# Optimization experiments

Hardware: AMD Instinct MI355X
Metric: run time of the kernel (lower is better)

The kernel has to match this reference:

```python
import jax, jax.numpy as jnp
import numpy as np

B, S, D, H, DFF = 4, 1024, 1024, 16, 4096
DK = D // H
EPS = 1e-9


def _layernorm(x, alpha, bias):
    # Faithful to source: torch.std is unbiased (ddof=1), eps added to std.
    mean = jnp.mean(x, axis=-1, keepdims=True)
    xc = x - mean
    std = jnp.sqrt(jnp.sum(xc * xc, axis=-1, keepdims=True) / (x.shape[-1] - 1))
    return alpha * xc / (std + EPS) + bias


def _mha(x, wq_w, wq_b, wo_w, wo_b):
    # Source bug preserved: w_q is used for q, k, AND v projections.
    p = (x @ wq_w + wq_b).reshape(B, S, H, DK).transpose(0, 2, 1, 3)  # [B,H,S,DK]
    scores = jnp.einsum('bhqd,bhkd->bhqk', p, p) / jnp.sqrt(jnp.asarray(DK, x.dtype))
    attn = jax.nn.softmax(scores, axis=-1)
    out = jnp.einsum('bhqk,bhkd->bhqd', attn, p)
    out = out.transpose(0, 2, 1, 3).reshape(B, S, D)
    return out @ wo_w + wo_b


def _ffn(x, w1, b1, w2, b2):
    return jax.nn.relu(x @ w1 + b1) @ w2 + b2


def setup_inputs() -> dict:
    key = jax.random.key(0)
    ks = jax.random.split(key, 8)
    sc = 0.02
    return {
        'x': jax.random.normal(ks[0], (B, S, D), jnp.float32),
        'wq_w': sc * jax.random.normal(ks[1], (D, D), jnp.float32),
        'wq_b': jnp.zeros((D,), jnp.float32),
        'wo_w': sc * jax.random.normal(ks[2], (D, D), jnp.float32),
        'wo_b': jnp.zeros((D,), jnp.float32),
        'ff1_w': sc * jax.random.normal(ks[3], (D, DFF), jnp.float32),
        'ff1_b': jnp.zeros((DFF,), jnp.float32),
        'ff2_w': sc * jax.random.normal(ks[4], (DFF, D), jnp.float32),
        'ff2_b': jnp.zeros((D,), jnp.float32),
        'alpha1': jnp.ones((1,), jnp.float32), 'bias1': jnp.zeros((1,), jnp.float32),
        'alpha2': jnp.ones((1,), jnp.float32), 'bias2': jnp.zeros((1,), jnp.float32),
        'alpha3': jnp.ones((1,), jnp.float32), 'bias3': jnp.zeros((1,), jnp.float32),
    }


def reference(x, wq_w, wq_b, wo_w, wo_b, ff1_w, ff1_b, ff2_w, ff2_b,
              alpha1, bias1, alpha2, bias2, alpha3, bias3):
    h1 = x + _mha(_layernorm(x, alpha1, bias1), wq_w, wq_b, wo_w, wo_b)
    h2 = h1 + _ffn(_layernorm(h1, alpha2, bias2), ff1_w, ff1_b, ff2_w, ff2_b)
    return _layernorm(h2, alpha3, bias3)
```

## Files before the change

### kernel.cpp

```cpp
#include <hip/hip_runtime.h>

typedef short short8 __attribute__((ext_vector_type(8)));
typedef float f32x4 __attribute__((ext_vector_type(4)));
typedef unsigned short u16x4 __attribute__((ext_vector_type(4)));

#define DEV static __device__ __forceinline__

DEV float b2f(unsigned short u) { return __uint_as_float(((unsigned)u) << 16); }
DEV unsigned short f2b(float f) {
    unsigned u = __float_as_uint(f);
    u += 0x7FFFu + ((u >> 16) & 1u);
    return (unsigned short)(u >> 16);
}
DEV float wred_sum(float v) {
#pragma unroll
    for (int o = 32; o; o >>= 1) v += __shfl_xor(v, o);
    return v;
}

DEV void gld_lds16(const unsigned short* g, unsigned short* l) {
    __builtin_amdgcn_global_load_lds((const __attribute__((address_space(1))) void*)g,
                                     (__attribute__((address_space(3))) void*)l, 16, 0, 0);
}

template <bool OUT_BF16>
__global__ __launch_bounds__(256) void ln_kernel(const float* __restrict__ in,
                                                 void* __restrict__ out_v,
                                                 const float* __restrict__ alpha_p,
                                                 const float* __restrict__ bias_p) {
    __shared__ float redA[4], redB[4];
    const int row = blockIdx.x;
    const int t = threadIdx.x;
    const int lane = t & 63, w = t >> 6;

    f32x4 xv = *(const f32x4*)&in[(size_t)row * 1024 + t * 4];

    float s = wred_sum(xv[0] + xv[1] + xv[2] + xv[3]);
    if (lane == 0) redA[w] = s;
    __syncthreads();
    float mean = (redA[0] + redA[1] + redA[2] + redA[3]) * (1.0f / 1024.0f);

    float d0 = xv[0] - mean, d1 = xv[1] - mean, d2 = xv[2] - mean, d3 = xv[3] - mean;
    float ss = wred_sum(d0 * d0 + d1 * d1 + d2 * d2 + d3 * d3);
    if (lane == 0) redB[w] = ss;
    __syncthreads();
    float var = (redB[0] + redB[1] + redB[2] + redB[3]) * (1.0f / 1023.0f);
    float denom = sqrtf(var) + 1e-9f;
    float inv = alpha_p[0] / denom;
    float bias = bias_p[0];

    if (OUT_BF16) {
        u16x4 o;
        o[0] = f2b(d0 * inv + bias);
        o[1] = f2b(d1 * inv + bias);
        o[2] = f2b(d2 * inv + bias);
        o[3] = f2b(d3 * inv + bias);
        *(u16x4*)&((unsigned short*)out_v)[(size_t)row * 1024 + t * 4] = o;
    } else {
        f32x4 o;
        o[0] = d0 * inv + bias;
        o[1] = d1 * inv + bias;
        o[2] = d2 * inv + bias;
        o[3] = d3 * inv + bias;
        *(f32x4*)&((float*)out_v)[(size_t)row * 1024 + t * 4] = o;
    }
}

__global__ __launch_bounds__(256) void transpose_cast_kernel(const float* __restrict__ in,
                                                             unsigned short* __restrict__ out,
                                                             int R, int C) {
    __shared__ unsigned short tile[32][33];
    const int c0 = blockIdx.x * 32, r0 = blockIdx.y * 32;
    const int x = threadIdx.x, y0 = threadIdx.y;
#pragma unroll
    for (int yy = y0; yy < 32; yy += 8) tile[yy][x] = f2b(in[(size_t)(r0 + yy) * C + c0 + x]);
    __syncthreads();
#pragma unroll
    for (int yy = y0; yy < 32; yy += 8) out[(size_t)(c0 + yy) * R + r0 + x] = tile[x][yy];
}

__global__ __launch_bounds__(256) void transpose_bf16_batch(const unsigned short* __restrict__ in,
                                                            unsigned short* __restrict__ out) {
    __shared__ unsigned short tile[32][33];
    const int b = blockIdx.z;
    const int d0 = blockIdx.x * 32, s0 = blockIdx.y * 32;
    const unsigned short* I = in + (size_t)b * 1024 * 1024;
    unsigned short* O = out + (size_t)b * 1024 * 1024;
    const int x = threadIdx.x, y0 = threadIdx.y;
#pragma unroll
    for (int yy = y0; yy < 32; yy += 8) tile[yy][x] = I[(size_t)(s0 + yy) * 1024 + d0 + x];
    __syncthreads();
#pragma unroll
    for (int yy = y0; yy < 32; yy += 8) O[(size_t)(d0 + yy) * 1024 + s0 + x] = tile[x][yy];
}

template <int BM, int BN, bool RELU, bool RES, bool OUT_BF16>
__global__ __launch_bounds__(256) void gemm2b(const unsigned short* __restrict__ A,
                                              const unsigned short* __restrict__ Bt,
                                              const float* __restrict__ bias,
                                              const float* __restrict__ res,
                                              void* __restrict__ C_v,
                                              int M, int N, int K) {
    constexpr int WM = BM / 2, WN = BN / 2;
    constexpr int FM = WM / 16, FN = WN / 16;
    __shared__ __align__(16) unsigned short As[3][BM * 64];
    __shared__ __align__(16) unsigned short Bs[3][BN * 64];

    const int t = threadIdx.x;
    const int lane = t & 63, w = t >> 6;
    const int wr = w >> 1, wc = w & 1;
    const int lr = lane & 15, g = lane >> 4;

    const int nwg = gridDim.x;
    const int cpx = nwg >> 3;
    const int wg = blockIdx.x;
    const int swz = (wg & 7) * cpx + (wg >> 3);
    const int NB = N / BN;
    const int m0 = (swz / NB) * BM, n0 = (swz % NB) * BN;

    f32x4 acc[FM][FN];
#pragma unroll
    for (int i = 0; i < FM; ++i)
#pragma unroll
        for (int j = 0; j < FN; ++j) acc[i][j] = (f32x4)0.0f;

    const int NT = K / 64;

#define STAGE2B(kt)                                                                        \
    {                                                                                      \
        const int buf_ = (kt) % 3;                                                         \
        const int k0_ = (kt) * 64;                                                         \
        _Pragma("unroll") for (int i = 0; i < BM / 32; ++i) {                              \
            int id = i * 256 + t;                                                          \
            int row = id >> 3, ch = (id & 7) ^ (row & 7);                                  \
            gld_lds16(&A[(size_t)(m0 + row) * K + k0_ + ch * 8],                           \
                      &As[buf_][(size_t)(i * 256 + (t & ~63)) * 8]);                       \
        }                                                                                  \
        _Pragma("unroll") for (int i = 0; i < BN / 32; ++i) {                              \
            int id = i * 256 + t;                                                          \
            int row = id >> 3, ch = (id & 7) ^ (row & 7);                                  \
            gld_lds16(&Bt[(size_t)(n0 + row) * K + k0_ + ch * 8],                          \
                      &Bs[buf_][(size_t)(i * 256 + (t & ~63)) * 8]);                       \
        }                                                                                  \
    }

    STAGE2B(0);
    STAGE2B(1);
    asm volatile("s_waitcnt vmcnt(6)" ::: "memory");
    __builtin_amdgcn_sched_barrier(0);
    __builtin_amdgcn_s_barrier();

    for (int kt = 0; kt < NT; ++kt) {
        const int buf = kt % 3;
        if (kt + 2 < NT) STAGE2B(kt + 2);

        short8 af[FM][2], bfr[FN][2];
#pragma unroll
        for (int mi = 0; mi < FM; ++mi) {
            int row = wr * WM + mi * 16 + lr;
#pragma unroll
            for (int ks = 0; ks < 2; ++ks) {
                int ch = (ks * 4 + g) ^ (row & 7);
                af[mi][ks] = *(const short8*)&As[buf][row * 64 + ch * 8];
            }
        }
#pragma unroll
        for (int ni = 0; ni < FN; ++ni) {
            int row = wc * WN + ni * 16 + lr;
#pragma unroll
            for (int ks = 0; ks < 2; ++ks) {
                int ch = (ks * 4 + g) ^ (row & 7);
                bfr[ni][ks] = *(const short8*)&Bs[buf][row * 64 + ch * 8];
            }
        }

        __builtin_amdgcn_s_setprio(1);
#pragma unroll
        for (int ks = 0; ks < 2; ++ks)
#pragma unroll
            for (int mi = 0; mi < FM; ++mi)
#pragma unroll
                for (int ni = 0; ni < FN; ++ni)
                    acc[mi][ni] = __builtin_amdgcn_mfma_f32_16x16x32_bf16(af[mi][ks], bfr[ni][ks], acc[mi][ni], 0, 0, 0);
        __builtin_amdgcn_s_setprio(0);

        if (kt + 2 < NT) {
            asm volatile("s_waitcnt vmcnt(6)" ::: "memory");
        } else if (kt + 1 < NT) {
            asm volatile("s_waitcnt vmcnt(0)" ::: "memory");
        }
        __builtin_amdgcn_sched_barrier(0);
        __builtin_amdgcn_s_barrier();
    }
#undef STAGE2B

    const int lg = g;
#pragma unroll
    for (int ni = 0; ni < FN; ++ni) {
        int col = n0 + wc * WN + ni * 16 + lr;
        float bv = bias[col];
#pragma unroll
        for (int mi = 0; mi < FM; ++mi) {
            int row0 = m0 + wr * WM + mi * 16 + lg * 4;
#pragma unroll
            for (int i = 0; i < 4; ++i) {
                int row = row0 + i;
                float x = acc[mi][ni][i] + bv;
                if (RES) x += res[(size_t)row * N + col];
                if (RELU) x = fmaxf(x, 0.0f);
                if (OUT_BF16)
                    ((unsigned short*)C_v)[(size_t)row * N + col] = f2b(x);
                else
                    ((float*)C_v)[(size_t)row * N + col] = x;
            }
        }
    }
}

template <bool RELU, bool OUT_BF16>
__global__ __launch_bounds__(512, 2) void gemm3(const unsigned short* __restrict__ A,
                                                const unsigned short* __restrict__ Bt,
                                                const float* __restrict__ bias,
                                                void* __restrict__ C_v,
                                                int M, int N, int K) {
    __shared__ __align__(16) unsigned short As[4][256 * 32];
    __shared__ __align__(16) unsigned short Bs[4][256 * 32];

    const int t = threadIdx.x;
    const int lane = t & 63;
    const int wid = t >> 6;
    const int wr = wid >> 2, wc = wid & 3;
    const int lr = lane & 15, g = lane >> 4;

    const int nwg = gridDim.x;
    const int cpx = nwg >> 3;
    const int wg = blockIdx.x;
    const int swz = (wg & 7) * cpx + (wg >> 3);
    const int NB = N / 256;
    const int m0 = (swz / NB) * 256, n0 = (swz % NB) * 256;

    f32x4 acc[8][4];
#pragma unroll
    for (int i = 0; i < 8; ++i)
#pragma unroll
        for (int j = 0; j < 4; ++j) acc[i][j] = (f32x4)0.0f;

    const int NT = K / 32;

#define STAGE3(kt)                                                                          \
    {                                                                                       \
        const int buf_ = (kt) & 3;                                                          \
        const int k0_ = (kt) * 32;                                                          \
        _Pragma("unroll") for (int s = 0; s < 2; ++s) {                                     \
            int id = s * 512 + t;                                                           \
            int row = id >> 2;                                                              \
            int ch = (id & 3) ^ ((row >> 1) & 3);                                           \
            gld_lds16(&A[(size_t)(m0 + row) * K + k0_ + ch * 8],                            \
                      &As[buf_][(size_t)(s * 512 + (t & ~63)) * 8]);                        \
            gld_lds16(&Bt[(size_t)(n0 + row) * K + k0_ + ch * 8],                           \
                      &Bs[buf_][(size_t)(s * 512 + (t & ~63)) * 8]);                        \
        }                                                                                   \
    }

    STAGE3(0);
    STAGE3(1);
    asm volatile("s_waitcnt vmcnt(4)" ::: "memory");
    __builtin_amdgcn_sched_barrier(0);
    __builtin_amdgcn_s_barrier();

    for (int kt = 0; kt < NT; ++kt) {
        const int buf = kt & 3;
        if (kt + 2 < NT) STAGE3(kt + 2);

        short8 af[8], bf[4];
#pragma unroll
        for (int mi = 0; mi < 8; ++mi) {
            int row = wr * 128 + mi * 16 + lr;
            int ch = g ^ ((row >> 1) & 3);
            af[mi] = *(const short8*)&As[buf][row * 32 + ch * 8];
        }
#pragma unroll
        for (int nj = 0; nj < 4; ++nj) {
            int row = wc * 64 + nj * 16 + lr;
            int ch = g ^ ((row >> 1) & 3);
            bf[nj] = *(const short8*)&Bs[buf][row * 32 + ch * 8];
        }

        __builtin_amdgcn_s_setprio(1);
#pragma unroll
        for (int mi = 0; mi < 8; ++mi)
#pragma unroll
            for (int nj = 0; nj < 4; ++nj)
                acc[mi][nj] = __builtin_amdgcn_mfma_f32_16x16x32_bf16(af[mi], bf[nj], acc[mi][nj], 0, 0, 0);
        __builtin_amdgcn_s_setprio(0);

        if (kt + 2 < NT) {
            asm volatile("s_waitcnt vmcnt(4)" ::: "memory");
        } else if (kt + 1 < NT) {
            asm volatile("s_waitcnt vmcnt(0)" ::: "memory");
        }
        __builtin_amdgcn_sched_barrier(0);
        __builtin_amdgcn_s_barrier();
    }
#undef STAGE3

#pragma unroll
    for (int nj = 0; nj < 4; ++nj) {
        int col = n0 + wc * 64 + nj * 16 + lr;
        float bv = bias[col];
#pragma unroll
        for (int mi = 0; mi < 8; ++mi) {
            int row0 = m0 + wr * 128 + mi * 16 + g * 4;
#pragma unroll
            for (int i = 0; i < 4; ++i) {
                int row = row0 + i;
                float x = acc[mi][nj][i] + bv;
                if (RELU) x = fmaxf(x, 0.0f);
                if (OUT_BF16)
                    ((unsigned short*)C_v)[(size_t)row * N + col] = f2b(x);
                else
                    ((float*)C_v)[(size_t)row * N + col] = x;
            }
        }
    }
}

__global__ __launch_bounds__(256) void attn_mfma_kernel(const unsigned short* __restrict__ p,
                                                        const unsigned short* __restrict__ pT,
                                                        unsigned short* __restrict__ out) {
    __shared__ __align__(16) unsigned short Ks[64 * 64];
    __shared__ __align__(16) unsigned short Vt[64 * 64];
    __shared__ __align__(16) unsigned short Ps[4 * 16 * 64];

    const int t = threadIdx.x;
    const int lane = t & 63, w = t >> 6;
    const int lr = lane & 15, g = lane >> 4;
    const int bh = blockIdx.x;
    const int qblk = blockIdx.y;
    const int b = bh >> 4, h = bh & 15;

    const unsigned short* Pm = p + (size_t)b * (1024 * 1024) + h * 64;
    const unsigned short* PT = pT + (size_t)b * (1024 * 1024) + (size_t)(h * 64) * 1024;

    const int q0 = qblk * 64 + w * 16;
    short8 qa0 = *(const short8*)&Pm[(size_t)(q0 + lr) * 1024 + g * 8];
    short8 qa1 = *(const short8*)&Pm[(size_t)(q0 + lr) * 1024 + 32 + g * 8];

    f32x4 acc[4];
#pragma unroll
    for (int i = 0; i < 4; ++i) acc[i] = (f32x4)0.0f;
    float mrow[4] = {-1e30f, -1e30f, -1e30f, -1e30f};
    float lsum[4] = {0.f, 0.f, 0.f, 0.f};

    unsigned short* Pw = &Ps[w * 16 * 64];

    for (int kt = 0; kt < 16; ++kt) {
        const int key0 = kt * 64;
        __syncthreads();
#pragma unroll
        for (int i = 0; i < 2; ++i) {
            int id = t + i * 256;
            int row = id >> 3, ch = (id & 7) * 8;
            int sw = ch ^ ((row & 7) << 3);
            short8 kv = *(const short8*)&Pm[(size_t)(key0 + row) * 1024 + ch];
            *(short8*)&Ks[row * 64 + sw] = kv;
            short8 vv = *(const short8*)&PT[(size_t)row * 1024 + key0 + ch];
            *(short8*)&Vt[row * 64 + sw] = vv;
        }
        __syncthreads();

        f32x4 s_acc[4];
#pragma unroll
        for (int kg = 0; kg < 4; ++kg) {
            s_acc[kg] = (f32x4)0.0f;
            int krow = kg * 16 + lr;
            int swz = (krow & 7) << 3;
            short8 kb0 = *(const short8*)&Ks[krow * 64 + ((g * 8) ^ swz)];
            short8 kb1 = *(const short8*)&Ks[krow * 64 + ((32 + g * 8) ^ swz)];
            s_acc[kg] = __builtin_amdgcn_mfma_f32_16x16x32_bf16(qa0, kb0, s_acc[kg], 0, 0, 0);
            s_acc[kg] = __builtin_amdgcn_mfma_f32_16x16x32_bf16(qa1, kb1, s_acc[kg], 0, 0, 0);
        }

#pragma unroll
        for (int reg = 0; reg < 4; ++reg) {
            float mx = fmaxf(fmaxf(s_acc[0][reg], s_acc[1][reg]),
                             fmaxf(s_acc[2][reg], s_acc[3][reg])) * 0.125f;
            mx = fmaxf(mx, __shfl_xor(mx, 1));
            mx = fmaxf(mx, __shfl_xor(mx, 2));
            mx = fmaxf(mx, __shfl_xor(mx, 4));
            mx = fmaxf(mx, __shfl_xor(mx, 8));
            float mnew = fmaxf(mrow[reg], mx);
            float scale = __expf(mrow[reg] - mnew);
            mrow[reg] = mnew;
            float psum = 0.f;
#pragma unroll
            for (int kg = 0; kg < 4; ++kg) {
                float pv = __expf(s_acc[kg][reg] * 0.125f - mnew);
                s_acc[kg][reg] = pv;
                psum += pv;
            }
            psum += __shfl_xor(psum, 1);
            psum += __shfl_xor(psum, 2);
            psum += __shfl_xor(psum, 4);
            psum += __shfl_xor(psum, 8);
            lsum[reg] = lsum[reg] * scale + psum;
#pragma unroll
            for (int dg = 0; dg < 4; ++dg) acc[dg][reg] *= scale;
        }

#pragma unroll
        for (int reg = 0; reg < 4; ++reg) {
            int q = g * 4 + reg;
            int swz = (q & 7) << 3;
#pragma unroll
            for (int kg = 0; kg < 4; ++kg) {
                int key = lr + 16 * kg;
                Pw[q * 64 + (key ^ swz)] = f2b(s_acc[kg][reg]);
            }
        }
        int pswz = (lr & 7) << 3;
        short8 pa0 = *(const short8*)&Pw[lr * 64 + ((g * 8) ^ pswz)];
        short8 pa1 = *(const short8*)&Pw[lr * 64 + ((32 + g * 8) ^ pswz)];

#pragma unroll
        for (int dg = 0; dg < 4; ++dg) {
            int drow = dg * 16 + lr;
            int swz = (drow & 7) << 3;
            short8 vb0 = *(const short8*)&Vt[drow * 64 + ((g * 8) ^ swz)];
            short8 vb1 = *(const short8*)&Vt[drow * 64 + ((32 + g * 8) ^ swz)];
            acc[dg] = __builtin_amdgcn_mfma_f32_16x16x32_bf16(pa0, vb0, acc[dg], 0, 0, 0);
            acc[dg] = __builtin_amdgcn_mfma_f32_16x16x32_bf16(pa1, vb1, acc[dg], 0, 0, 0);
        }
    }

    unsigned short* O = out + (size_t)b * (1024 * 1024) + h * 64;
#pragma unroll
    for (int reg = 0; reg < 4; ++reg) {
        float inv = 1.0f / lsum[reg];
        int q = q0 + g * 4 + reg;
#pragma unroll
        for (int dg = 0; dg < 4; ++dg) {
            O[(size_t)q * 1024 + dg * 16 + lr] = f2b(acc[dg][reg] * inv);
        }
    }
}

extern "C" void kernel_launch(void* const* d_in, const int* in_sizes, int n_in,
                              void* d_out, int out_size, void* d_ws, size_t ws_size,
                              hipStream_t stream) {
    const float* x = (const float*)d_in[0];
    const float* wq_w = (const float*)d_in[1];
    const float* wq_b = (const float*)d_in[2];
    const float* wo_w = (const float*)d_in[3];
    const float* wo_b = (const float*)d_in[4];
    const float* ff1_w = (const float*)d_in[5];
    const float* ff1_b = (const float*)d_in[6];
    const float* ff2_w = (const float*)d_in[7];
    const float* ff2_b = (const float*)d_in[8];
    const float* alpha1 = (const float*)d_in[9];
    const float* bias1 = (const float*)d_in[10];
    const float* alpha2 = (const float*)d_in[11];
    const float* bias2 = (const float*)d_in[12];
    const float* alpha3 = (const float*)d_in[13];
    const float* bias3 = (const float*)d_in[14];
    float* out = (float*)d_out;

    const size_t MB = 1u << 20;
    char* ws = (char*)d_ws;
    unsigned short* wq_t = (unsigned short*)(ws + 0 * MB);
    unsigned short* wo_t = (unsigned short*)(ws + 2 * MB);
    unsigned short* ff1_t = (unsigned short*)(ws + 4 * MB);
    unsigned short* ff2_t = (unsigned short*)(ws + 12 * MB);
    unsigned short* lnbuf = (unsigned short*)(ws + 20 * MB);
    unsigned short* pbuf = (unsigned short*)(ws + 28 * MB);
    unsigned short* attn = (unsigned short*)(ws + 36 * MB);
    float* h1 = (float*)(ws + 44 * MB);
    unsigned short* pbT = (unsigned short*)(ws + 60 * MB);
    unsigned short* mid = (unsigned short*)(ws + 60 * MB);
    float* h2 = (float*)(ws + 28 * MB);

    const int M = 4096;

    transpose_cast_kernel<<<dim3(32, 32), dim3(32, 8), 0, stream>>>(wq_w, wq_t, 1024, 1024);
    transpose_cast_kernel<<<dim3(32, 32), dim3(32, 8), 0, stream>>>(wo_w, wo_t, 1024, 1024);
    transpose_cast_kernel<<<dim3(128, 32), dim3(32, 8), 0, stream>>>(ff1_w, ff1_t, 1024, 4096);
    transpose_cast_kernel<<<dim3(32, 128), dim3(32, 8), 0, stream>>>(ff2_w, ff2_t, 4096, 1024);

    ln_kernel<true><<<M, 256, 0, stream>>>(x, lnbuf, alpha1, bias1);
    gemm2b<128, 64, false, false, true><<<512, 256, 0, stream>>>(lnbuf, wq_t, wq_b, nullptr, pbuf, M, 1024, 1024);
    transpose_bf16_batch<<<dim3(32, 32, 4), dim3(32, 8), 0, stream>>>(pbuf, pbT);
    attn_mfma_kernel<<<dim3(64, 16), 256, 0, stream>>>(pbuf, pbT, attn);
    gemm2b<128, 64, false, true, false><<<512, 256, 0, stream>>>(attn, wo_t, wo_b, x, h1, M, 1024, 1024);
    ln_kernel<true><<<M, 256, 0, stream>>>(h1, lnbuf, alpha2, bias2);
    gemm3<true, true><<<256, 512, 0, stream>>>(lnbuf, ff1_t, ff1_b, mid, M, 4096, 1024);
    gemm2b<128, 64, false, true, false><<<512, 256, 0, stream>>>(mid, ff2_t, ff2_b, h1, h2, M, 1024, 4096);
    ln_kernel<false><<<M, 256, 0, stream>>>(h2, out, alpha3, bias3);
}
```

Before: 251.2 us.

## Merge weight casts with first layernorm and shrink FFN1 GEMM tile to 256x128

The four weight transpose-cast launches and the first layernorm are merged into one prelude kernel that dispatches on block index, cutting launch overhead and letting the independent work overlap. The FFN1 GEMM moves from 256x256 tiles with 4 LDS buffers to 256x128 tiles with 3 buffers. That doubles the grid to 512 workgroups and requests 4 waves-per-SIMD occupancy to fill the CUs better. The trade-off is less B-operand reuse per tile, and the higher occupancy target may put pressure on registers.

```diff
diff --git a/kernel.cpp b/kernel.cpp
--- a/kernel.cpp
+++ b/kernel.cpp
@@ -66,17 +66,61 @@
     }
 }
 
-__global__ __launch_bounds__(256) void transpose_cast_kernel(const float* __restrict__ in,
-                                                             unsigned short* __restrict__ out,
-                                                             int R, int C) {
+__global__ __launch_bounds__(256) void prelude_kernel(
+    const float* __restrict__ x, unsigned short* __restrict__ lnbuf,
+    const float* __restrict__ alpha1, const float* __restrict__ bias1,
+    const float* __restrict__ wq_w, unsigned short* __restrict__ wq_t,
+    const float* __restrict__ wo_w, unsigned short* __restrict__ wo_t,
+    const float* __restrict__ ff1_w, unsigned short* __restrict__ ff1_t,
+    const float* __restrict__ ff2_w, unsigned short* __restrict__ ff2_t) {
     __shared__ unsigned short tile[32][33];
-    const int c0 = blockIdx.x * 32, r0 = blockIdx.y * 32;
-    const int x = threadIdx.x, y0 = threadIdx.y;
-#pragma unroll
-    for (int yy = y0; yy < 32; yy += 8) tile[yy][x] = f2b(in[(size_t)(r0 + yy) * C + c0 + x]);
+    __shared__ float redA[4], redB[4];
+    const int t = threadIdx.x;
+    int bid = blockIdx.x;
+
+    if (bid < 4096) {
+        const int row = bid;
+        const int lane = t & 63, w = t >> 6;
+        f32x4 xv = *(const f32x4*)&x[(size_t)row * 1024 + t * 4];
+        float s = wred_sum(xv[0] + xv[1] + xv[2] + xv[3]);
+        if (lane == 0) redA[w] = s;
+        __syncthreads();
+        float mean = (redA[0] + redA[1] + redA[2] + redA[3]) * (1.0f / 1024.0f);
+        float d0 = xv[0] - mean, d1 = xv[1] - mean, d2 = xv[2] - mean, d3 = xv[3] - mean;
+        float ss = wred_sum(d0 * d0 + d1 * d1 + d2 * d2 + d3 * d3);
+        if (lane == 0) redB[w] = ss;
+        __syncthreads();
+        float var = (redB[0] + redB[1] + redB[2] + redB[3]) * (1.0f / 1023.0f);
+        float inv = alpha1[0] / (sqrtf(var) + 1e-9f);
+        float bias = bias1[0];
+        u16x4 o;
+        o[0] = f2b(d0 * inv + bias);
+        o[1] = f2b(d1 * inv + bias);
+        o[2] = f2b(d2 * inv + bias);
+        o[3] = f2b(d3 * inv + bias);
+        *(u16x4*)&lnbuf[(size_t)row * 1024 + t * 4] = o;
+        return;
+    }
+    bid -= 4096;
+    const float* src;
+    unsigned short* dst;
+    int R, C, gx;
+    if (bid < 1024) {
+        src = wq_w; dst = wq_t; R = 1024; C = 1024; gx = 32;
+    } else if (bid < 2048) {
+        bid -= 1024; src = wo_w; dst = wo_t; R = 1024; C = 1024; gx = 32;
+    } else if (bid < 6144) {
+        bid -= 2048; src = ff1_w; dst = ff1_t; R = 1024; C = 4096; gx = 128;
+    } else {
+        bid -= 6144; src = ff2_w; dst = ff2_t; R = 4096; C = 1024; gx = 32;
+    }
+    const int c0 = (bid % gx) * 32, r0 = (bid / gx) * 32;
+    const int xx = t & 31, y0 = t >> 5;
+#pragma unroll
+    for (int yy = y0; yy < 32; yy += 8) tile[yy][xx] = f2b(src[(size_t)(r0 + yy) * C + c0 + xx]);
     __syncthreads();
 #pragma unroll
-    for (int yy = y0; yy < 32; yy += 8) out[(size_t)(c0 + yy) * R + r0 + x] = tile[x][yy];
+    for (int yy = y0; yy < 32; yy += 8) dst[(size_t)(c0 + yy) * R + r0 + xx] = tile[xx][yy];
 }
 
 __global__ __launch_bounds__(256) void transpose_bf16_batch(const unsigned short* __restrict__ in,
@@ -218,38 +262,38 @@
 }
 
 template <bool RELU, bool OUT_BF16>
-__global__ __launch_bounds__(512, 2) void gemm3(const unsigned short* __restrict__ A,
-                                                const unsigned short* __restrict__ Bt,
-                                                const float* __restrict__ bias,
-                                                void* __restrict__ C_v,
-                                                int M, int N, int K) {
-    __shared__ __align__(16) unsigned short As[4][256 * 32];
-    __shared__ __align__(16) unsigned short Bs[4][256 * 32];
+__global__ __launch_bounds__(512, 4) void gemm3b(const unsigned short* __restrict__ A,
+                                                 const unsigned short* __restrict__ Bt,
+                                                 const float* __restrict__ bias,
+                                                 void* __restrict__ C_v,
+                                                 int M, int N, int K) {
+    __shared__ __align__(16) unsigned short As[3][256 * 32];
+    __shared__ __align__(16) unsigned short Bs[3][128 * 32];
 
     const int t = threadIdx.x;
     const int lane = t & 63;
     const int wid = t >> 6;
-    const int wr = wid >> 2, wc = wid & 3;
+    const int wr = wid >> 1, wc = wid & 1;
     const int lr = lane & 15, g = lane >> 4;
 
     const int nwg = gridDim.x;
     const int cpx = nwg >> 3;
     const int wg = blockIdx.x;
     const int swz = (wg & 7) * cpx + (wg >> 3);
-    const int NB = N / 256;
-    const int m0 = (swz / NB) * 256, n0 = (swz % NB) * 256;
-
-    f32x4 acc[8][4];
-#pragma unroll
-    for (int i = 0; i < 8; ++i)
+    const int NB = N / 128;
+    const int m0 = (swz / NB) * 256, n0 = (swz % NB) * 128;
+
+    f32x4 acc[4][4];
+#pragma unroll
+    for (int i = 0; i < 4; ++i)
 #pragma unroll
         for (int j = 0; j < 4; ++j) acc[i][j] = (f32x4)0.0f;
 
     const int NT = K / 32;
 
-#define STAGE3(kt)                                                                          \
+#define STAGE3B(kt)                                                                         \
     {                                                                                       \
-        const int buf_ = (kt) & 3;                                                          \
+        const int buf_ = (kt) % 3;                                                          \
         const int k0_ = (kt) * 32;                                                          \
         _Pragma("unroll") for (int s = 0; s < 2; ++s) {                                     \
             int id = s * 512 + t;                                                           \
@@ -257,25 +301,29 @@
             int ch = (id & 3) ^ ((row >> 1) & 3);                                           \
             gld_lds16(&A[(size_t)(m0 + row) * K + k0_ + ch * 8],                            \
                       &As[buf_][(size_t)(s * 512 + (t & ~63)) * 8]);                        \
+        }                                                                                   \
+        {                                                                                   \
+            int row = t >> 2;                                                               \
+            int ch = (t & 3) ^ ((row >> 1) & 3);                                            \
             gld_lds16(&Bt[(size_t)(n0 + row) * K + k0_ + ch * 8],                           \
-                      &Bs[buf_][(size_t)(s * 512 + (t & ~63)) * 8]);                        \
+                      &Bs[buf_][(size_t)(t & ~63) * 8]);                                    \
         }                                                                                   \
     }
 
-    STAGE3(0);
-    STAGE3(1);
-    asm volatile("s_waitcnt vmcnt(4)" ::: "memory");
+    STAGE3B(0);
+    STAGE3B(1);
+    asm volatile("s_waitcnt vmcnt(3)" ::: "memory");
     __builtin_amdgcn_sched_barrier(0);
     __builtin_amdgcn_s_barrier();
 
     for (int kt = 0; kt < NT; ++kt) {
-        const int buf = kt & 3;
-        if (kt + 2 < NT) STAGE3(kt + 2);
-
-        short8 af[8], bf[4];
-#pragma unroll
-        for (int mi = 0; mi < 8; ++mi) {
-            int row = wr * 128 + mi * 16 + lr;
+        const int buf = kt % 3;
+        if (kt + 2 < NT) STAGE3B(kt + 2);
+
+        short8 af[4], bf[4];
+#pragma unroll
+        for (int mi = 0; mi < 4; ++mi) {
+            int row = wr * 64 + mi * 16 + lr;
             int ch = g ^ ((row >> 1) & 3);
             af[mi] = *(const short8*)&As[buf][row * 32 + ch * 8];
         }
@@ -288,29 +336,29 @@
 
         __builtin_amdgcn_s_setprio(1);
 #pragma unroll
-        for (int mi = 0; mi < 8; ++mi)
+        for (int mi = 0; mi < 4; ++mi)
 #pragma unroll
             for (int nj = 0; nj < 4; ++nj)
                 acc[mi][nj] = __builtin_amdgcn_mfma_f32_16x16x32_bf16(af[mi], bf[nj], acc[mi][nj], 0, 0, 0);
         __builtin_amdgcn_s_setprio(0);
 
         if (kt + 2 < NT) {
-            asm volatile("s_waitcnt vmcnt(4)" ::: "memory");
+            asm volatile("s_waitcnt vmcnt(3)" ::: "memory");
         } else if (kt + 1 < NT) {
             asm volatile("s_waitcnt vmcnt(0)" ::: "memory");
         }
         __builtin_amdgcn_sched_barrier(0);
         __builtin_amdgcn_s_barrier();
     }
-#undef STAGE3
+#undef STAGE3B
 
 #pragma unroll
     for (int nj = 0; nj < 4; ++nj) {
         int col = n0 + wc * 64 + nj * 16 + lr;
         float bv = bias[col];
 #pragma unroll
-        for (int mi = 0; mi < 8; ++mi) {
-            int row0 = m0 + wr * 128 + mi * 16 + g * 4;
+        for (int mi = 0; mi < 4; ++mi) {
+            int row0 = m0 + wr * 64 + mi * 16 + g * 4;
 #pragma unroll
             for (int i = 0; i < 4; ++i) {
                 int row = row0 + i;
@@ -481,18 +529,15 @@
 
     const int M = 4096;
 
-    transpose_cast_kernel<<<dim3(32, 32), dim3(32, 8), 0, stream>>>(wq_w, wq_t, 1024, 1024);
-    transpose_cast_kernel<<<dim3(32, 32), dim3(32, 8), 0, stream>>>(wo_w, wo_t, 1024, 1024);
-    transpose_cast_kernel<<<dim3(128, 32), dim3(32, 8), 0, stream>>>(ff1_w, ff1_t, 1024, 4096);
-    transpose_cast_kernel<<<dim3(32, 128), dim3(32, 8), 0, stream>>>(ff2_w, ff2_t, 4096, 1024);
-
-    ln_kernel<true><<<M, 256, 0, stream>>>(x, lnbuf, alpha1, bias1);
+    prelude_kernel<<<14336, 256, 0, stream>>>(x, lnbuf, alpha1, bias1,
+                                              wq_w, wq_t, wo_w, wo_t,
+                                              ff1_w, ff1_t, ff2_w, ff2_t);
     gemm2b<128, 64, false, false, true><<<512, 256, 0, stream>>>(lnbuf, wq_t, wq_b, nullptr, pbuf, M, 1024, 1024);
     transpose_bf16_batch<<<dim3(32, 32, 4), dim3(32, 8), 0, stream>>>(pbuf, pbT);
     attn_mfma_kernel<<<dim3(64, 16), 256, 0, stream>>>(pbuf, pbT, attn);
     gemm2b<128, 64, false, true, false><<<512, 256, 0, stream>>>(attn, wo_t, wo_b, x, h1, M, 1024, 1024);
     ln_kernel<true><<<M, 256, 0, stream>>>(h1, lnbuf, alpha2, bias2);
-    gemm3<true, true><<<256, 512, 0, stream>>>(lnbuf, ff1_t, ff1_b, mid, M, 4096, 1024);
+    gemm3b<true, true><<<512, 512, 0, stream>>>(lnbuf, ff1_t, ff1_b, mid, M, 4096, 1024);
     gemm2b<128, 64, false, true, false><<<512, 256, 0, stream>>>(mid, ff2_t, ff2_b, h1, h2, M, 1024, 4096);
     ln_kernel<false><<<M, 256, 0, stream>>>(h2, out, alpha3, bias3);
 }
```

Measured after the change: 233.0 us. 7.3% less time.
